# Optimization experiments

Hardware: AMD Instinct MI355X
Metric: run time of the kernel (lower is better)

## Reference

```python
import jax, jax.numpy as jnp
import numpy as np

NUM_CLASSES = 11


def setup_inputs() -> dict:
    key = jax.random.key(0)
    k1, k2 = jax.random.split(key)
    x = jax.random.uniform(k1, (16, 3, 512, 512), dtype=jnp.float32)
    y = jax.random.randint(k2, (16, 1, 512, 512), 0, NUM_CLASSES, dtype=jnp.int64)
    return {"x": x, "y": y}


def reference(x, y):
    b, c, h, w = x.shape
    xm = jnp.mean(x, axis=1, keepdims=True)          # (b,1,h,w) channel-mean brightness
    a1 = jnp.zeros((b, h, w), dtype=x.dtype)         # zeros fallback, as in the torch code
    d = jnp.zeros((), dtype=x.dtype)
    for i in range(NUM_CLASSES):
        # NOTE: (b,1,h,w) where-args broadcast against (b,h,w)->(1,b,h,w),
        # producing (b,b,h,w) exactly as torch does.
        a2 = jnp.where(y == i, xm, a1)
        d2 = jnp.mean(a2)                            # scalar mean incl. zeros
        a2 = jnp.where(a2 == 0, d2, a2)              # replace zeros by the mean
        d3 = jnp.mean((a2 - d2) ** 2)                # variance-like term
        d = d + d3
    return d
```

## Files before the change

kernel.cpp:

```cpp
#include <hip/hip_runtime.h>
#include <hip/hip_fp16.h>


constexpr int kHW = 512 * 512;
constexpr int kB = 16;
constexpr int kNPix = kB * kHW;
constexpr int kNCls = 11;
constexpr int kNQ = 2 * kNCls + 1;
constexpr int kBlocks = 1024;
constexpr int kThreads = 256;

__global__ __launch_bounds__(kThreads) void seg_main_kernel(
    const float* __restrict__ x, const int* __restrict__ y,
    double* __restrict__ pd) {
  const int tid = threadIdx.x, bid = blockIdx.x;

  __half2 acc[6];
#pragma unroll
  for (int r = 0; r < 6; ++r) acc[r] = __builtin_bit_cast(__half2, 0u);
  unsigned long long pack = 0ull;
  float ss = 0.f;

  constexpr int kStride = kBlocks * kThreads;
  constexpr int kIters = (kNPix / 4) / kStride;
#pragma unroll
  for (int it = 0; it < kIters; ++it) {
    const int g = bid * kThreads + tid + it * kStride;
    const int p = g << 2;
    const int b = p >> 18;
    const int off = p & (kHW - 1);
    const float* xb = x + (size_t)b * 3 * kHW + off;
    const float4 x0 = *reinterpret_cast<const float4*>(xb);
    const float4 x1 = *reinterpret_cast<const float4*>(xb + kHW);
    const float4 x2 = *reinterpret_cast<const float4*>(xb + 2 * kHW);
    const int4 yv = *reinterpret_cast<const int4*>(y + p);

    const float sv4[4] = {x0.x + x1.x + x2.x, x0.y + x1.y + x2.y,
                          x0.z + x1.z + x2.z, x0.w + x1.w + x2.w};
    const int yy[4] = {yv.x, yv.y, yv.z, yv.w};
#pragma unroll
    for (int j = 0; j < 4; ++j) {
      const float sv = sv4[j];
      ss = fmaf(sv, sv, ss);
      const int cls = (sv != 0.f) ? yy[j] : 11;
      const unsigned long long oh = 0x3C00ull << ((cls & 3) << 4);
      const unsigned lo = (unsigned)oh, hi = (unsigned)(oh >> 32);
      const int w = cls >> 2;
      unsigned pr0 = (w == 0) ? lo : 0u, pr1 = (w == 0) ? hi : 0u;
      unsigned pr2 = (w == 1) ? lo : 0u, pr3 = (w == 1) ? hi : 0u;
      unsigned pr4 = (w == 2) ? lo : 0u, pr5 = (w == 2) ? hi : 0u;
      const __half2 m2 = __half2half2(__float2half(sv));
      acc[0] = __hfma2(__builtin_bit_cast(__half2, pr0), m2, acc[0]);
      acc[1] = __hfma2(__builtin_bit_cast(__half2, pr1), m2, acc[1]);
      acc[2] = __hfma2(__builtin_bit_cast(__half2, pr2), m2, acc[2]);
      acc[3] = __hfma2(__builtin_bit_cast(__half2, pr3), m2, acc[3]);
      acc[4] = __hfma2(__builtin_bit_cast(__half2, pr4), m2, acc[4]);
      acc[5] = __hfma2(__builtin_bit_cast(__half2, pr5), m2, acc[5]);
      pack += 1ull << (5 * cls);
    }
  }

  float qv[kNQ];
#pragma unroll
  for (int r = 0; r < 6; ++r) {
    const float2 f2 = __half22float2(acc[r]);
    if (2 * r < kNCls) qv[2 * r] = f2.x;
    if (2 * r + 1 < kNCls) qv[2 * r + 1] = f2.y;
  }
#pragma unroll
  for (int i = 0; i < kNCls; ++i)
    qv[kNCls + i] = (float)((unsigned)(pack >> (5 * i)) & 31u);
  qv[2 * kNCls] = ss;

  __shared__ float arr[kNQ][kThreads];
#pragma unroll
  for (int q = 0; q < kNQ; ++q) arr[q][tid] = qv[q];
  __syncthreads();

  if (tid < kNQ * 8) {
    const int q = tid >> 3, l = tid & 7;
    const float4* row = reinterpret_cast<const float4*>(arr[q]);
    double dv = 0.0;
#pragma unroll
    for (int jj = 0; jj < kThreads / 32; ++jj) {
      const float4 v = row[l + 8 * jj];
      dv += (double)((v.x + v.y) + (v.z + v.w));
    }
#pragma unroll
    for (int o = 4; o > 0; o >>= 1) dv += __shfl_down(dv, o, 8);
    if (l == 0) pd[(size_t)q * kBlocks + bid] = dv;
  }
}

__global__ __launch_bounds__(1024) void seg_final_kernel(
    const double* __restrict__ pd, float* __restrict__ out) {
  __shared__ double tot[kNQ];
  const int q = threadIdx.x >> 5;
  const int lane = threadIdx.x & 31;
  if (q < kNQ) {
    double v = 0.0;
#pragma unroll
    for (int j = 0; j < kBlocks / 32; ++j)
      v += pd[(size_t)q * kBlocks + lane + 32 * j];
#pragma unroll
    for (int o = 16; o > 0; o >>= 1) v += __shfl_down(v, o, 32);
    if (lane == 0) tot[q] = v;
  }
  __syncthreads();
  if (threadIdx.x == 0) {
    const double N = (double)kNPix;
    double acc2 = tot[2 * kNCls] / 9.0;
    for (int i = 0; i < kNCls; ++i) {
      const double S = tot[i] / 3.0;
      const double C = tot[kNCls + i];
      acc2 += S * S * (C / N - 2.0) / N;
    }
    out[0] = (float)(acc2 / N);
  }
}

extern "C" void kernel_launch(void* const* d_in, const int* in_sizes, int n_in,
                              void* d_out, int out_size, void* d_ws, size_t ws_size,
                              hipStream_t stream) {
  const float* x = (const float*)d_in[0];
  const int* y = (const int*)d_in[1];
  float* out = (float*)d_out;
  double* pd = (double*)d_ws;

  seg_main_kernel<<<kBlocks, kThreads, 0, stream>>>(x, y, pd);
  seg_final_kernel<<<1, 1024, 0, stream>>>(pd, out);
}
```

Baseline: 22.13 us.

## Replace fp16 class-sum accumulators with fixed-point integer packing and contiguous block tiles

Per-class brightness sums are now quantized to fixed-point (scale 256) and accumulated as packed 16-bit lanes inside 32-bit integers with plain integer adds, replacing half2 FMAs. Each block now handles one contiguous 4096-pixel tile of a single image, so it no longer uses a grid-stride index. Block partials are stored as floats and read with vectorized float4 loads in the final kernel. The packed 16-bit lanes can overflow or carry into the neighbouring lane if a class sum gets large, and the quantization adds rounding error.

```diff
diff --git a/kernel.cpp b/kernel.cpp
--- a/kernel.cpp
+++ b/kernel.cpp
@@ -1,5 +1,4 @@
 #include <hip/hip_runtime.h>
-#include <hip/hip_fp16.h>
 
 
 constexpr int kHW = 512 * 512;
@@ -9,53 +8,43 @@
 constexpr int kNQ = 2 * kNCls + 1;
 constexpr int kBlocks = 1024;
 constexpr int kThreads = 256;
+constexpr int kIters = 4;
 
 __global__ __launch_bounds__(kThreads) void seg_main_kernel(
     const float* __restrict__ x, const int* __restrict__ y,
-    double* __restrict__ pd) {
+    float* __restrict__ pd) {
   const int tid = threadIdx.x, bid = blockIdx.x;
+  const int b = bid >> 6;
+  const int basePix = (bid & 63) << 12;
+  const float* xb = x + (size_t)b * 3 * kHW + basePix;
+  const int* yb = y + (size_t)b * kHW + basePix;
 
-  __half2 acc[6];
-#pragma unroll
-  for (int r = 0; r < 6; ++r) acc[r] = __builtin_bit_cast(__half2, 0u);
+  unsigned acc[6] = {0u, 0u, 0u, 0u, 0u, 0u};
   unsigned long long pack = 0ull;
   float ss = 0.f;
 
-  constexpr int kStride = kBlocks * kThreads;
-  constexpr int kIters = (kNPix / 4) / kStride;
 #pragma unroll
   for (int it = 0; it < kIters; ++it) {
-    const int g = bid * kThreads + tid + it * kStride;
-    const int p = g << 2;
-    const int b = p >> 18;
-    const int off = p & (kHW - 1);
-    const float* xb = x + (size_t)b * 3 * kHW + off;
-    const float4 x0 = *reinterpret_cast<const float4*>(xb);
-    const float4 x1 = *reinterpret_cast<const float4*>(xb + kHW);
-    const float4 x2 = *reinterpret_cast<const float4*>(xb + 2 * kHW);
-    const int4 yv = *reinterpret_cast<const int4*>(y + p);
+    const int o = (it << 10) + (tid << 2);
+    const float4 x0 = *reinterpret_cast<const float4*>(xb + o);
+    const float4 x1 = *reinterpret_cast<const float4*>(xb + kHW + o);
+    const float4 x2 = *reinterpret_cast<const float4*>(xb + 2 * kHW + o);
+    const int4 yv = *reinterpret_cast<const int4*>(yb + o);
 
-    const float sv4[4] = {x0.x + x1.x + x2.x, x0.y + x1.y + x2.y,
-                          x0.z + x1.z + x2.z, x0.w + x1.w + x2.w};
+    const float sv4[4] = {(x0.x + x1.x) + x2.x, (x0.y + x1.y) + x2.y,
+                          (x0.z + x1.z) + x2.z, (x0.w + x1.w) + x2.w};
     const int yy[4] = {yv.x, yv.y, yv.z, yv.w};
 #pragma unroll
     for (int j = 0; j < 4; ++j) {
       const float sv = sv4[j];
       ss = fmaf(sv, sv, ss);
-      const int cls = (sv != 0.f) ? yy[j] : 11;
-      const unsigned long long oh = 0x3C00ull << ((cls & 3) << 4);
-      const unsigned lo = (unsigned)oh, hi = (unsigned)(oh >> 32);
-      const int w = cls >> 2;
-      unsigned pr0 = (w == 0) ? lo : 0u, pr1 = (w == 0) ? hi : 0u;
-      unsigned pr2 = (w == 1) ? lo : 0u, pr3 = (w == 1) ? hi : 0u;
-      unsigned pr4 = (w == 2) ? lo : 0u, pr5 = (w == 2) ? hi : 0u;
-      const __half2 m2 = __half2half2(__float2half(sv));
-      acc[0] = __hfma2(__builtin_bit_cast(__half2, pr0), m2, acc[0]);
-      acc[1] = __hfma2(__builtin_bit_cast(__half2, pr1), m2, acc[1]);
-      acc[2] = __hfma2(__builtin_bit_cast(__half2, pr2), m2, acc[2]);
-      acc[3] = __hfma2(__builtin_bit_cast(__half2, pr3), m2, acc[3]);
-      acc[4] = __hfma2(__builtin_bit_cast(__half2, pr4), m2, acc[4]);
-      acc[5] = __hfma2(__builtin_bit_cast(__half2, pr5), m2, acc[5]);
+      const int cls = (sv != 0.f) ? yy[j] : 12;
+      const unsigned q = (unsigned)fmaf(sv, 256.f, 0.5f);
+      const unsigned qsh = q << ((cls & 1) << 4);
+      const int r = cls >> 1;
+#pragma unroll
+      for (int rr = 0; rr < 6; ++rr)
+        acc[rr] += (r == rr) ? qsh : 0u;
       pack += 1ull << (5 * cls);
     }
   }
@@ -63,9 +52,9 @@
   float qv[kNQ];
 #pragma unroll
   for (int r = 0; r < 6; ++r) {
-    const float2 f2 = __half22float2(acc[r]);
-    if (2 * r < kNCls) qv[2 * r] = f2.x;
-    if (2 * r + 1 < kNCls) qv[2 * r + 1] = f2.y;
+    const unsigned lo = acc[r] & 0xFFFFu, hi = acc[r] >> 16;
+    qv[2 * r] = (float)lo;
+    if (2 * r + 1 < kNCls) qv[2 * r + 1] = (float)hi;
   }
 #pragma unroll
   for (int i = 0; i < kNCls; ++i)
@@ -80,28 +69,31 @@
   if (tid < kNQ * 8) {
     const int q = tid >> 3, l = tid & 7;
     const float4* row = reinterpret_cast<const float4*>(arr[q]);
-    double dv = 0.0;
+    float fv = 0.f;
 #pragma unroll
     for (int jj = 0; jj < kThreads / 32; ++jj) {
       const float4 v = row[l + 8 * jj];
-      dv += (double)((v.x + v.y) + (v.z + v.w));
+      fv += ((v.x + v.y) + (v.z + v.w));
     }
 #pragma unroll
-    for (int o = 4; o > 0; o >>= 1) dv += __shfl_down(dv, o, 8);
-    if (l == 0) pd[(size_t)q * kBlocks + bid] = dv;
+    for (int o = 4; o > 0; o >>= 1) fv += __shfl_down(fv, o, 8);
+    if (l == 0) pd[(size_t)q * kBlocks + bid] = fv;
   }
 }
 
 __global__ __launch_bounds__(1024) void seg_final_kernel(
-    const double* __restrict__ pd, float* __restrict__ out) {
+    const float* __restrict__ pd, float* __restrict__ out) {
   __shared__ double tot[kNQ];
   const int q = threadIdx.x >> 5;
   const int lane = threadIdx.x & 31;
   if (q < kNQ) {
+    const float4* row = reinterpret_cast<const float4*>(pd + (size_t)q * kBlocks);
     double v = 0.0;
 #pragma unroll
-    for (int j = 0; j < kBlocks / 32; ++j)
-      v += pd[(size_t)q * kBlocks + lane + 32 * j];
+    for (int j = 0; j < kBlocks / 128; ++j) {
+      const float4 f = row[lane + 32 * j];
+      v += (double)((f.x + f.y) + (f.z + f.w));
+    }
 #pragma unroll
     for (int o = 16; o > 0; o >>= 1) v += __shfl_down(v, o, 32);
     if (lane == 0) tot[q] = v;
@@ -111,7 +103,7 @@
     const double N = (double)kNPix;
     double acc2 = tot[2 * kNCls] / 9.0;
     for (int i = 0; i < kNCls; ++i) {
-      const double S = tot[i] / 3.0;
+      const double S = tot[i] / 768.0;
       const double C = tot[kNCls + i];
       acc2 += S * S * (C / N - 2.0) / N;
     }
@@ -125,7 +117,7 @@
   const float* x = (const float*)d_in[0];
   const int* y = (const int*)d_in[1];
   float* out = (float*)d_out;
-  double* pd = (double*)d_ws;
+  float* pd = (float*)d_ws;
 
   seg_main_kernel<<<kBlocks, kThreads, 0, stream>>>(x, y, pd);
   seg_final_kernel<<<1, 1024, 0, stream>>>(pd, out);
```

New measurement: 19.30 us. -12.8%, faster.
